# Performance work log

Hardware: AMD Instinct MI355X
Metric: run time of the kernel (lower is better)

## Reference

```python
import jax, jax.numpy as jnp
import numpy as np

N = 100000   # nodes
E = 1000000  # edges
DIN = 64
DH = 128     # num_hidden == out_dim
EPS = 1e-5


def setup_inputs() -> dict:
    key = jax.random.key(0)
    ks = jax.random.split(key, 16)
    x = jax.random.normal(ks[0], (N, DIN), jnp.float32)
    src = jax.random.randint(ks[1], (E,), 0, N)
    dst = jax.random.randint(ks[2], (E,), 0, N)
    dims = [(DIN, DH), (DH, DH), (DH, DH)]
    inp = {"x": x, "src": src, "dst": dst}
    for l, (di, do) in enumerate(dims):
        s = 1.0 / np.sqrt(di)
        inp[f"w_self{l}"] = jax.random.normal(ks[3 + 4 * l], (di, do), jnp.float32) * s
        inp[f"w_neigh{l}"] = jax.random.normal(ks[4 + 4 * l], (di, do), jnp.float32) * s
        inp[f"b{l}"] = jnp.zeros((do,), jnp.float32)
    # layernorm affine params for layers 0 and 1 (last layer has norm=None)
    for l in (0, 1):
        inp[f"g{l}"] = jnp.ones((DH,), jnp.float32)
        inp[f"be{l}"] = jnp.zeros((DH,), jnp.float32)
    return inp


def _layernorm(h, g, b):
    mu = jnp.mean(h, axis=-1, keepdims=True)
    var = jnp.mean(jnp.square(h - mu), axis=-1, keepdims=True)
    return (h - mu) * jax.lax.rsqrt(var + EPS) * g + b


def _sage_layer(h, src, dst, w_self, w_neigh, b, gamma, beta):
    # mean aggregation over incoming edges (DGL copy_u + mean)
    msg = h[src]                                            # [E, d_in]
    agg = jax.ops.segment_sum(msg, dst, num_segments=N)     # [N, d_in]
    deg = jax.ops.segment_sum(jnp.ones((E,), h.dtype), dst, num_segments=N)
    h_neigh = agg / jnp.where(deg > 0, deg, 1.0)[:, None]
    out = h @ w_self + h_neigh @ w_neigh + b
    out = jax.nn.relu(out)  # DGL applies activation before norm
    if gamma is not None:
        out = _layernorm(out, gamma, beta)
    return out


def reference(x, src, dst,
              w_self0, w_neigh0, b0,
              w_self1, w_neigh1, b1,
              w_self2, w_neigh2, b2,
              g0, be0, g1, be1):
    h = x  # dropout is identity in eval mode
    h = _sage_layer(h, src, dst, w_self0, w_neigh0, b0, g0, be0)
    h = _sage_layer(h, src, dst, w_self1, w_neigh1, b1, g1, be1)
    h = _sage_layer(h, src, dst, w_self2, w_neigh2, b2, None, None)
    return h
```

## Files before the change

### kernel.cpp

```cpp
#include <hip/hip_runtime.h>

#define NN   100000
#define NE   1000000
#define EPS  1e-5f
#define CAP  40

typedef unsigned short ushort_t;
typedef unsigned int   uint_t;
typedef __attribute__((ext_vector_type(8))) __bf16 bf16x8;
typedef __attribute__((ext_vector_type(4))) float  f32x4;

static __device__ __forceinline__ ushort_t f2bf(float f) {
    uint_t u = __float_as_uint(f);
    u = u + 0x7fff + ((u >> 16) & 1);
    return (ushort_t)(u >> 16);
}
static __device__ __forceinline__ float bf2f(uint_t us) {
    return __uint_as_float(us << 16);
}

__global__ __launch_bounds__(256) void k_fill(const int* __restrict__ src,
                                              const int* __restrict__ dst,
                                              int* __restrict__ cnt,
                                              int* __restrict__ slots) {
    int e = blockIdx.x * 256 + threadIdx.x;
    if (e >= NE) return;
    int d   = dst[e];
    int pos = atomicAdd(&cnt[d], 1);
    if (pos < CAP) slots[d * CAP + pos] = src[e];
}

__global__ __launch_bounds__(256) void k_xprep(const float* __restrict__ x,
                                               ushort_t* __restrict__ xb) {
    int i = blockIdx.x * 256 + threadIdx.x;
    if (i >= NN * 32) return;
    float2 v = *(const float2*)(x + (size_t)i * 2);
    uint_t pk = (uint_t)f2bf(v.x) | ((uint_t)f2bf(v.y) << 16);
    *(uint_t*)(xb + (size_t)i * 2) = pk;
}

__global__ __launch_bounds__(256) void k_wprep(const float* __restrict__ wsf,
                                               const float* __restrict__ wng,
                                               __bf16* __restrict__ Bt, int DIN) {
    int K = 2 * DIN;
    int idx = blockIdx.x * 256 + threadIdx.x;
    if (idx >= 128 * K) return;
    int col = idx / K;
    int k   = idx % K;
    float v = (k < DIN) ? wsf[k * 128 + col] : wng[(k - DIN) * 128 + col];
    Bt[idx] = (__bf16)v;
}

template <int DIN>
__global__ __launch_bounds__(256) void k_gather(const ushort_t* __restrict__ h,
                                                const int* __restrict__ slots,
                                                const int* __restrict__ cnt,
                                                ushort_t* __restrict__ aggm) {
    constexpr int EL = (DIN == 64) ? 4 : 8;
    int lane = threadIdx.x & 63;
    int wid  = threadIdx.x >> 6;
    int node = blockIdx.x * 4 + wid;
    if (node >= NN) return;
    int deg = cnt[node];
    int c   = deg < CAP ? deg : CAP;
    int q   = lane >> 4;
    int l16 = lane & 15;

    float acc[EL];
#pragma unroll
    for (int k = 0; k < EL; ++k) acc[k] = 0.f;

    if (c > 0) {
        const int* sl = slots + (size_t)node * CAP;
        int iv = sl[lane < c ? lane : c - 1];
        for (int j = 0; j < c; j += 16) {
#pragma unroll
            for (int t = 0; t < 4; ++t) {
                int r = j + t * 4 + q;
                int s = __shfl(iv, (r < c ? r : c - 1));
                if (r < c) {
                    if (DIN == 64) {
                        uint2 v = *(const uint2*)(h + (size_t)s * 64 + l16 * 4);
                        acc[0] += bf2f(v.x & 0xffffu);
                        acc[1] += bf2f(v.x >> 16);
                        acc[2] += bf2f(v.y & 0xffffu);
                        acc[3] += bf2f(v.y >> 16);
                    } else {
                        uint4 v = *(const uint4*)(h + (size_t)s * 128 + l16 * 8);
                        acc[0] += bf2f(v.x & 0xffffu); acc[1] += bf2f(v.x >> 16);
                        acc[2] += bf2f(v.y & 0xffffu); acc[3] += bf2f(v.y >> 16);
                        acc[4] += bf2f(v.z & 0xffffu); acc[5] += bf2f(v.z >> 16);
                        acc[6] += bf2f(v.w & 0xffffu); acc[7] += bf2f(v.w >> 16);
                    }
                }
            }
        }
    }
#pragma unroll
    for (int k = 0; k < EL; ++k) {
        acc[k] += __shfl_xor(acc[k], 16);
        acc[k] += __shfl_xor(acc[k], 32);
    }
    if (lane < 16) {
        float inv = 1.0f / (float)(deg > 0 ? deg : 1);
        if (DIN == 64) {
            uint2 o;
            o.x = (uint_t)f2bf(acc[0] * inv) | ((uint_t)f2bf(acc[1] * inv) << 16);
            o.y = (uint_t)f2bf(acc[2] * inv) | ((uint_t)f2bf(acc[3] * inv) << 16);
            *(uint2*)(aggm + (size_t)node * 64 + lane * 4) = o;
        } else {
            uint4 o;
            o.x = (uint_t)f2bf(acc[0] * inv) | ((uint_t)f2bf(acc[1] * inv) << 16);
            o.y = (uint_t)f2bf(acc[2] * inv) | ((uint_t)f2bf(acc[3] * inv) << 16);
            o.z = (uint_t)f2bf(acc[4] * inv) | ((uint_t)f2bf(acc[5] * inv) << 16);
            o.w = (uint_t)f2bf(acc[6] * inv) | ((uint_t)f2bf(acc[7] * inv) << 16);
            *(uint4*)(aggm + (size_t)node * 128 + lane * 8) = o;
        }
    }
}

template <int DIN, bool DO_LN, bool OUT_F32>
__global__ __launch_bounds__(256) void k_gemm_mfma(const ushort_t* __restrict__ ha,
                                                   const ushort_t* __restrict__ aggm,
                                                   const __bf16* __restrict__ Bt,
                                                   const float* __restrict__ bias,
                                                   const float* __restrict__ gamma,
                                                   const float* __restrict__ beta,
                                                   void* __restrict__ out) {
    constexpr int K   = 2 * DIN;
    constexpr int KS2 = DIN / 32;
    int lane = threadIdx.x & 63;
    int w    = threadIdx.x >> 6;
    int n16  = lane & 15;
    int q    = lane >> 4;
    int base = blockIdx.x * 64;

    __shared__ float C[64 * 132];

    bf16x8 Bs[2][KS2][2];
#pragma unroll
    for (int hh = 0; hh < 2; ++hh)
#pragma unroll
        for (int ks = 0; ks < KS2; ++ks)
#pragma unroll
            for (int ct = 0; ct < 2; ++ct) {
                int col = w * 32 + ct * 16 + n16;
                int k   = hh * DIN + ks * 32 + q * 8;
                Bs[hh][ks][ct] = *(const bf16x8*)(Bt + (size_t)col * K + k);
            }

    int rowc[4];
#pragma unroll
    for (int ng = 0; ng < 4; ++ng) {
        int row  = base + ng * 16 + n16;
        rowc[ng] = row < NN ? row : NN - 1;
    }

    f32x4 acc[4][2] = {};

#pragma unroll
    for (int ks = 0; ks < KS2; ++ks) {
        bf16x8 a[4];
#pragma unroll
        for (int ng = 0; ng < 4; ++ng)
            a[ng] = *(const bf16x8*)(ha + (size_t)rowc[ng] * DIN + ks * 32 + q * 8);
#pragma unroll
        for (int ng = 0; ng < 4; ++ng)
#pragma unroll
            for (int ct = 0; ct < 2; ++ct)
                acc[ng][ct] = __builtin_amdgcn_mfma_f32_16x16x32_bf16(
                    a[ng], Bs[0][ks][ct], acc[ng][ct], 0, 0, 0);
    }
#pragma unroll
    for (int ks = 0; ks < KS2; ++ks) {
        bf16x8 a[4];
#pragma unroll
        for (int ng = 0; ng < 4; ++ng)
            a[ng] = *(const bf16x8*)(aggm + (size_t)rowc[ng] * DIN + ks * 32 + q * 8);
#pragma unroll
        for (int ng = 0; ng < 4; ++ng)
#pragma unroll
            for (int ct = 0; ct < 2; ++ct)
                acc[ng][ct] = __builtin_amdgcn_mfma_f32_16x16x32_bf16(
                    a[ng], Bs[1][ks][ct], acc[ng][ct], 0, 0, 0);
    }

#pragma unroll
    for (int ng = 0; ng < 4; ++ng)
#pragma unroll
        for (int ct = 0; ct < 2; ++ct) {
            int col = w * 32 + ct * 16 + n16;
            float bv = bias[col];
#pragma unroll
            for (int r = 0; r < 4; ++r) {
                float v = acc[ng][ct][r] + bv;
                C[(ng * 16 + q * 4 + r) * 132 + col] = fmaxf(v, 0.f);
            }
        }
    __syncthreads();

    for (int rr = 0; rr < 16; ++rr) {
        int lrow = w * 16 + rr;
        int node = base + lrow;
        if (node >= NN) break;
        float a0 = C[lrow * 132 + lane];
        float a1 = C[lrow * 132 + 64 + lane];
        float o0 = a0, o1 = a1;
        if (DO_LN) {
            float s = a0 + a1, qq = a0 * a0 + a1 * a1;
#pragma unroll
            for (int m = 1; m < 64; m <<= 1) {
                s  += __shfl_xor(s, m);
                qq += __shfl_xor(qq, m);
            }
            float mu  = s * (1.f / 128.f);
            float var = qq * (1.f / 128.f) - mu * mu;
            float rs  = rsqrtf(var + EPS);
            o0 = (a0 - mu) * rs * gamma[lane]      + beta[lane];
            o1 = (a1 - mu) * rs * gamma[64 + lane] + beta[64 + lane];
        }
        if (OUT_F32) {
            ((float*)out)[(size_t)node * 128 + lane]      = o0;
            ((float*)out)[(size_t)node * 128 + 64 + lane] = o1;
        } else {
            ((ushort_t*)out)[(size_t)node * 128 + lane]      = f2bf(o0);
            ((ushort_t*)out)[(size_t)node * 128 + 64 + lane] = f2bf(o1);
        }
    }
}

extern "C" void kernel_launch(void* const* d_in, const int* in_sizes, int n_in,
                              void* d_out, int out_size, void* d_ws, size_t ws_size,
                              hipStream_t stream) {
    const float* x   = (const float*)d_in[0];
    const int*   src = (const int*)d_in[1];
    const int*   dst = (const int*)d_in[2];
    const float* ws0 = (const float*)d_in[3];
    const float* wn0 = (const float*)d_in[4];
    const float* b0  = (const float*)d_in[5];
    const float* ws1 = (const float*)d_in[6];
    const float* wn1 = (const float*)d_in[7];
    const float* b1  = (const float*)d_in[8];
    const float* ws2 = (const float*)d_in[9];
    const float* wn2 = (const float*)d_in[10];
    const float* b2  = (const float*)d_in[11];
    const float* g0  = (const float*)d_in[12];
    const float* be0 = (const float*)d_in[13];
    const float* g1  = (const float*)d_in[14];
    const float* be1 = (const float*)d_in[15];
    (void)in_sizes; (void)n_in; (void)out_size; (void)ws_size;

    char*  ws  = (char*)d_ws;
    size_t off = 0;
    auto alloc = [&](size_t bytes) -> void* {
        void* p = ws + off;
        off = (off + bytes + 255) & ~(size_t)255;
        return p;
    };
    ushort_t* xb     = (ushort_t*)alloc((size_t)NN * 64 * 2);
    ushort_t* h1b    = (ushort_t*)alloc((size_t)NN * 128 * 2);
    ushort_t* h2b    = (ushort_t*)alloc((size_t)NN * 128 * 2);
    ushort_t* aggm   = (ushort_t*)alloc((size_t)NN * 128 * 2);
    int*      slots  = (int*)alloc((size_t)NN * CAP * 4);
    int*      cnt    = (int*)alloc((size_t)NN * 4);
    __bf16*   Bt0    = (__bf16*)alloc(128 * 128 * 2);
    __bf16*   Bt1    = (__bf16*)alloc(128 * 256 * 2);
    __bf16*   Bt2    = (__bf16*)alloc(128 * 256 * 2);

    const int EB = (NE + 255) / 256;
    const int AB = (NN + 3) / 4;
    const int GB = (NN + 63) / 64;
    const int XB = (NN * 32 + 255) / 256;

    hipMemsetAsync(cnt, 0, (size_t)NN * 4, stream);
    k_fill<<<EB, 256, 0, stream>>>(src, dst, cnt, slots);
    k_xprep<<<XB, 256, 0, stream>>>(x, xb);
    k_wprep<<<64, 256, 0, stream>>>(ws0, wn0, Bt0, 64);
    k_wprep<<<128, 256, 0, stream>>>(ws1, wn1, Bt1, 128);
    k_wprep<<<128, 256, 0, stream>>>(ws2, wn2, Bt2, 128);

    k_gather<64><<<AB, 256, 0, stream>>>(xb, slots, cnt, aggm);
    k_gemm_mfma<64, true, false><<<GB, 256, 0, stream>>>(xb, aggm, Bt0, b0, g0, be0, h1b);

    k_gather<128><<<AB, 256, 0, stream>>>(h1b, slots, cnt, aggm);
    k_gemm_mfma<128, true, false><<<GB, 256, 0, stream>>>(h1b, aggm, Bt1, b1, g1, be1, h2b);

    k_gather<128><<<AB, 256, 0, stream>>>(h2b, slots, cnt, aggm);
    k_gemm_mfma<128, false, true><<<GB, 256, 0, stream>>>(h2b, aggm, Bt2, b2, nullptr, nullptr, d_out);
}
```

Baseline: 438.8 us.

## Fuse neighbor gather into MFMA GEMM kernel via shared-memory aggregate tile

Merges the per-layer gather kernel into the GEMM kernel. Each wave aggregates 16 nodes' neighbor means into an LDS tile, which then feeds the neighbor-half MFMAs directly instead of going through a global aggm buffer. This removes the global write and re-read of the aggregate and drops three kernel launches. In exchange each block now does gather and GEMM serially, with fewer independent waves in flight to hide gather latency, and more LDS per block, which may lower occupancy.

```diff
diff --git a/kernel.cpp b/kernel.cpp
--- a/kernel.cpp
+++ b/kernel.cpp
@@ -51,91 +51,27 @@
     Bt[idx] = (__bf16)v;
 }
 
-template <int DIN>
-__global__ __launch_bounds__(256) void k_gather(const ushort_t* __restrict__ h,
-                                                const int* __restrict__ slots,
-                                                const int* __restrict__ cnt,
-                                                ushort_t* __restrict__ aggm) {
-    constexpr int EL = (DIN == 64) ? 4 : 8;
-    int lane = threadIdx.x & 63;
-    int wid  = threadIdx.x >> 6;
-    int node = blockIdx.x * 4 + wid;
-    if (node >= NN) return;
-    int deg = cnt[node];
-    int c   = deg < CAP ? deg : CAP;
-    int q   = lane >> 4;
-    int l16 = lane & 15;
-
-    float acc[EL];
-#pragma unroll
-    for (int k = 0; k < EL; ++k) acc[k] = 0.f;
-
-    if (c > 0) {
-        const int* sl = slots + (size_t)node * CAP;
-        int iv = sl[lane < c ? lane : c - 1];
-        for (int j = 0; j < c; j += 16) {
-#pragma unroll
-            for (int t = 0; t < 4; ++t) {
-                int r = j + t * 4 + q;
-                int s = __shfl(iv, (r < c ? r : c - 1));
-                if (r < c) {
-                    if (DIN == 64) {
-                        uint2 v = *(const uint2*)(h + (size_t)s * 64 + l16 * 4);
-                        acc[0] += bf2f(v.x & 0xffffu);
-                        acc[1] += bf2f(v.x >> 16);
-                        acc[2] += bf2f(v.y & 0xffffu);
-                        acc[3] += bf2f(v.y >> 16);
-                    } else {
-                        uint4 v = *(const uint4*)(h + (size_t)s * 128 + l16 * 8);
-                        acc[0] += bf2f(v.x & 0xffffu); acc[1] += bf2f(v.x >> 16);
-                        acc[2] += bf2f(v.y & 0xffffu); acc[3] += bf2f(v.y >> 16);
-                        acc[4] += bf2f(v.z & 0xffffu); acc[5] += bf2f(v.z >> 16);
-                        acc[6] += bf2f(v.w & 0xffffu); acc[7] += bf2f(v.w >> 16);
-                    }
-                }
-            }
-        }
-    }
-#pragma unroll
-    for (int k = 0; k < EL; ++k) {
-        acc[k] += __shfl_xor(acc[k], 16);
-        acc[k] += __shfl_xor(acc[k], 32);
-    }
-    if (lane < 16) {
-        float inv = 1.0f / (float)(deg > 0 ? deg : 1);
-        if (DIN == 64) {
-            uint2 o;
-            o.x = (uint_t)f2bf(acc[0] * inv) | ((uint_t)f2bf(acc[1] * inv) << 16);
-            o.y = (uint_t)f2bf(acc[2] * inv) | ((uint_t)f2bf(acc[3] * inv) << 16);
-            *(uint2*)(aggm + (size_t)node * 64 + lane * 4) = o;
-        } else {
-            uint4 o;
-            o.x = (uint_t)f2bf(acc[0] * inv) | ((uint_t)f2bf(acc[1] * inv) << 16);
-            o.y = (uint_t)f2bf(acc[2] * inv) | ((uint_t)f2bf(acc[3] * inv) << 16);
-            o.z = (uint_t)f2bf(acc[4] * inv) | ((uint_t)f2bf(acc[5] * inv) << 16);
-            o.w = (uint_t)f2bf(acc[6] * inv) | ((uint_t)f2bf(acc[7] * inv) << 16);
-            *(uint4*)(aggm + (size_t)node * 128 + lane * 8) = o;
-        }
-    }
-}
-
 template <int DIN, bool DO_LN, bool OUT_F32>
-__global__ __launch_bounds__(256) void k_gemm_mfma(const ushort_t* __restrict__ ha,
-                                                   const ushort_t* __restrict__ aggm,
-                                                   const __bf16* __restrict__ Bt,
-                                                   const float* __restrict__ bias,
-                                                   const float* __restrict__ gamma,
-                                                   const float* __restrict__ beta,
-                                                   void* __restrict__ out) {
-    constexpr int K   = 2 * DIN;
-    constexpr int KS2 = DIN / 32;
+__global__ __launch_bounds__(256) void k_fused(const ushort_t* __restrict__ h,
+                                               const int* __restrict__ slots,
+                                               const int* __restrict__ cnt,
+                                               const __bf16* __restrict__ Bt,
+                                               const float* __restrict__ bias,
+                                               const float* __restrict__ gamma,
+                                               const float* __restrict__ beta,
+                                               void* __restrict__ out) {
+    constexpr int K    = 2 * DIN;
+    constexpr int KS2  = DIN / 32;
+    constexpr int ASTR = DIN + 8;
+    constexpr int EL   = DIN / 16;
     int lane = threadIdx.x & 63;
     int w    = threadIdx.x >> 6;
     int n16  = lane & 15;
     int q    = lane >> 4;
     int base = blockIdx.x * 64;
 
-    __shared__ float C[64 * 132];
+    __shared__ ushort_t AG[64 * ASTR];
+    __shared__ float    C[64 * 132];
 
     bf16x8 Bs[2][KS2][2];
 #pragma unroll
@@ -149,6 +85,62 @@
                 Bs[hh][ks][ct] = *(const bf16x8*)(Bt + (size_t)col * K + k);
             }
 
+    for (int rr = 0; rr < 16; ++rr) {
+        int node  = base + w * 16 + rr;
+        int nodec = node < NN ? node : NN - 1;
+        int deg   = cnt[nodec];
+        int c     = deg < CAP ? deg : CAP;
+        float ga[EL];
+#pragma unroll
+        for (int k2 = 0; k2 < EL; ++k2) ga[k2] = 0.f;
+        if (c > 0) {
+            const int* sl = slots + (size_t)nodec * CAP;
+            int iv = sl[lane < c ? lane : c - 1];
+            for (int j = 0; j < c; j += 16) {
+#pragma unroll
+                for (int t = 0; t < 4; ++t) {
+                    int r = j + t * 4 + q;
+                    int s = __shfl(iv, (r < c ? r : c - 1));
+                    if (r < c) {
+                        if (DIN == 64) {
+                            uint2 v = *(const uint2*)(h + (size_t)s * 64 + n16 * 4);
+                            ga[0] += bf2f(v.x & 0xffffu); ga[1] += bf2f(v.x >> 16);
+                            ga[2] += bf2f(v.y & 0xffffu); ga[3] += bf2f(v.y >> 16);
+                        } else {
+                            uint4 v = *(const uint4*)(h + (size_t)s * 128 + n16 * 8);
+                            ga[0] += bf2f(v.x & 0xffffu); ga[1] += bf2f(v.x >> 16);
+                            ga[2] += bf2f(v.y & 0xffffu); ga[3] += bf2f(v.y >> 16);
+                            ga[4] += bf2f(v.z & 0xffffu); ga[5] += bf2f(v.z >> 16);
+                            ga[6] += bf2f(v.w & 0xffffu); ga[7] += bf2f(v.w >> 16);
+                        }
+                    }
+                }
+            }
+        }
+#pragma unroll
+        for (int k2 = 0; k2 < EL; ++k2) {
+            ga[k2] += __shfl_xor(ga[k2], 16);
+            ga[k2] += __shfl_xor(ga[k2], 32);
+        }
+        if (lane < 16) {
+            float inv = 1.0f / (float)(deg > 0 ? deg : 1);
+            ushort_t* dp = AG + (w * 16 + rr) * ASTR + n16 * EL;
+            if (DIN == 64) {
+                uint2 o;
+                o.x = (uint_t)f2bf(ga[0] * inv) | ((uint_t)f2bf(ga[1] * inv) << 16);
+                o.y = (uint_t)f2bf(ga[2] * inv) | ((uint_t)f2bf(ga[3] * inv) << 16);
+                *(uint2*)dp = o;
+            } else {
+                uint4 o;
+                o.x = (uint_t)f2bf(ga[0] * inv) | ((uint_t)f2bf(ga[1] * inv) << 16);
+                o.y = (uint_t)f2bf(ga[2] * inv) | ((uint_t)f2bf(ga[3] * inv) << 16);
+                o.z = (uint_t)f2bf(ga[4] * inv) | ((uint_t)f2bf(ga[5] * inv) << 16);
+                o.w = (uint_t)f2bf(ga[6] * inv) | ((uint_t)f2bf(ga[7] * inv) << 16);
+                *(uint4*)dp = o;
+            }
+        }
+    }
+
     int rowc[4];
 #pragma unroll
     for (int ng = 0; ng < 4; ++ng) {
@@ -156,34 +148,39 @@
         rowc[ng] = row < NN ? row : NN - 1;
     }
 
-    f32x4 acc[4][2] = {};
+    f32x4 cacc[4][2] = {};
 
 #pragma unroll
     for (int ks = 0; ks < KS2; ++ks) {
         bf16x8 a[4];
 #pragma unroll
         for (int ng = 0; ng < 4; ++ng)
-            a[ng] = *(const bf16x8*)(ha + (size_t)rowc[ng] * DIN + ks * 32 + q * 8);
+            a[ng] = *(const bf16x8*)(h + (size_t)rowc[ng] * DIN + ks * 32 + q * 8);
 #pragma unroll
         for (int ng = 0; ng < 4; ++ng)
 #pragma unroll
             for (int ct = 0; ct < 2; ++ct)
-                acc[ng][ct] = __builtin_amdgcn_mfma_f32_16x16x32_bf16(
-                    a[ng], Bs[0][ks][ct], acc[ng][ct], 0, 0, 0);
-    }
+                cacc[ng][ct] = __builtin_amdgcn_mfma_f32_16x16x32_bf16(
+                    a[ng], Bs[0][ks][ct], cacc[ng][ct], 0, 0, 0);
+    }
+
+    __syncthreads();
+
 #pragma unroll
     for (int ks = 0; ks < KS2; ++ks) {
         bf16x8 a[4];
 #pragma unroll
         for (int ng = 0; ng < 4; ++ng)
-            a[ng] = *(const bf16x8*)(aggm + (size_t)rowc[ng] * DIN + ks * 32 + q * 8);
+            a[ng] = *(const bf16x8*)(AG + (ng * 16 + n16) * ASTR + ks * 32 + q * 8);
 #pragma unroll
         for (int ng = 0; ng < 4; ++ng)
 #pragma unroll
             for (int ct = 0; ct < 2; ++ct)
-                acc[ng][ct] = __builtin_amdgcn_mfma_f32_16x16x32_bf16(
-                    a[ng], Bs[1][ks][ct], acc[ng][ct], 0, 0, 0);
-    }
+                cacc[ng][ct] = __builtin_amdgcn_mfma_f32_16x16x32_bf16(
+                    a[ng], Bs[1][ks][ct], cacc[ng][ct], 0, 0, 0);
+    }
+
+    __syncthreads();
 
 #pragma unroll
     for (int ng = 0; ng < 4; ++ng)
@@ -193,7 +190,7 @@
             float bv = bias[col];
 #pragma unroll
             for (int r = 0; r < 4; ++r) {
-                float v = acc[ng][ct][r] + bv;
+                float v = cacc[ng][ct][r] + bv;
                 C[(ng * 16 + q * 4 + r) * 132 + col] = fmaxf(v, 0.f);
             }
         }
@@ -260,7 +257,6 @@
     ushort_t* xb     = (ushort_t*)alloc((size_t)NN * 64 * 2);
     ushort_t* h1b    = (ushort_t*)alloc((size_t)NN * 128 * 2);
     ushort_t* h2b    = (ushort_t*)alloc((size_t)NN * 128 * 2);
-    ushort_t* aggm   = (ushort_t*)alloc((size_t)NN * 128 * 2);
     int*      slots  = (int*)alloc((size_t)NN * CAP * 4);
     int*      cnt    = (int*)alloc((size_t)NN * 4);
     __bf16*   Bt0    = (__bf16*)alloc(128 * 128 * 2);
@@ -268,7 +264,6 @@
     __bf16*   Bt2    = (__bf16*)alloc(128 * 256 * 2);
 
     const int EB = (NE + 255) / 256;
-    const int AB = (NN + 3) / 4;
     const int GB = (NN + 63) / 64;
     const int XB = (NN * 32 + 255) / 256;
 
@@ -279,12 +274,7 @@
     k_wprep<<<128, 256, 0, stream>>>(ws1, wn1, Bt1, 128);
     k_wprep<<<128, 256, 0, stream>>>(ws2, wn2, Bt2, 128);
 
-    k_gather<64><<<AB, 256, 0, stream>>>(xb, slots, cnt, aggm);
-    k_gemm_mfma<64, true, false><<<GB, 256, 0, stream>>>(xb, aggm, Bt0, b0, g0, be0, h1b);
-
-    k_gather<128><<<AB, 256, 0, stream>>>(h1b, slots, cnt, aggm);
-    k_gemm_mfma<128, true, false><<<GB, 256, 0, stream>>>(h1b, aggm, Bt1, b1, g1, be1, h2b);
-
-    k_gather<128><<<AB, 256, 0, stream>>>(h2b, slots, cnt, aggm);
-    k_gemm_mfma<128, false, true><<<GB, 256, 0, stream>>>(h2b, aggm, Bt2, b2, nullptr, nullptr, d_out);
-}
+    k_fused<64, true, false><<<GB, 256, 0, stream>>>(xb, slots, cnt, Bt0, b0, g0, be0, h1b);
+    k_fused<128, true, false><<<GB, 256, 0, stream>>>(h1b, slots, cnt, Bt1, b1, g1, be1, h2b);
+    k_fused<128, false, true><<<GB, 256, 0, stream>>>(h2b, slots, cnt, Bt2, b2, nullptr, nullptr, d_out);
+}
```

New measurement: 555.3 us. +26.5%, slower.
